# Kernel optimization log

Hardware: AMD Instinct MI355X
Metric: run time of the kernel (lower is better)

## Reference

```python
import jax, jax.numpy as jnp
import numpy as np

B, S, D = 4, 2048, 512
H = 8
DEPTH = D // H  # 64


def setup_inputs() -> dict:
    key = jax.random.key(0)
    ks = jax.random.split(key, 6)
    scale = 1.0 / np.sqrt(D)
    return {
        "x": jax.random.normal(ks[0], (B, S, D), dtype=jnp.float32),
        "y": jax.random.normal(ks[1], (B, S, D), dtype=jnp.float32),
        "W_q": jax.random.normal(ks[2], (D, D), dtype=jnp.float32) * scale,
        "W_k": jax.random.normal(ks[3], (D, D), dtype=jnp.float32) * scale,
        "W_v": jax.random.normal(ks[4], (D, D), dtype=jnp.float32) * scale,
        "W_o": jax.random.normal(ks[5], (D, D), dtype=jnp.float32) * scale,
    }


def _split_heads(t):
    # [B, S, D] -> [B, H, S, DEPTH]
    b, s, _ = t.shape
    return t.reshape(b, s, H, DEPTH).transpose(0, 2, 1, 3)


def reference(x, y, W_q, W_k, W_v, W_o):
    q = _split_heads(x @ W_q) * (DEPTH ** -0.5)   # [B,H,Sq,d]
    k = _split_heads(y @ W_k)                      # [B,H,Sk,d]
    v = _split_heads(y @ W_v)                      # [B,H,Sk,d]
    logits = jnp.einsum("bhqd,bhkd->bhqk", q, k)   # [B,H,Sq,Sk]
    weights = jax.nn.softmax(logits, axis=-1)
    attn = jnp.einsum("bhqk,bhkd->bhqd", weights, v)  # [B,H,Sq,d]
    attn = attn.transpose(0, 2, 1, 3).reshape(x.shape[0], x.shape[1], D)
    return attn @ W_o
```

## Files before the change

kernel.cpp:

```cpp
#include <hip/hip_runtime.h>
#include <hip/hip_bf16.h>
#include <math.h>
#include <stdint.h>

#define NB 4
#define NS 2048
#define ND 512
#define NH 8
#define DEP 64
#define KVHALF (NS / 2)

typedef __attribute__((ext_vector_type(8))) short bf16x8;
typedef __attribute__((ext_vector_type(4))) short bf16x4;
typedef __attribute__((ext_vector_type(4))) float f32x4;
typedef __attribute__((ext_vector_type(16))) float f32x16;

#define QSCALE 0.18033688011112042f

__device__ __forceinline__ short f2b(float f) {
  unsigned u = __float_as_uint(f);
  u += 0x7FFF + ((u >> 16) & 1);
  return (short)(u >> 16);
}
__device__ __forceinline__ unsigned pk2(float a, float b) {
  union { __hip_bfloat162 h; unsigned u; } c;
  c.h = __float22bfloat162_rn(float2{a, b});
  return c.u;
}
__device__ __forceinline__ void dma16(const void* g, void* l) {
  __builtin_amdgcn_global_load_lds(
      (const __attribute__((address_space(1))) void*)g,
      (__attribute__((address_space(3))) void*)l, 16, 0, 0);
}

__global__ __launch_bounds__(256) void prep(
    const float* __restrict__ x, const float* __restrict__ y,
    const float* __restrict__ W0, const float* __restrict__ W1,
    const float* __restrict__ W2, const float* __restrict__ W3,
    short* __restrict__ xb, short* __restrict__ yb, short* __restrict__ T0,
    short* __restrict__ T1, short* __restrict__ T2, short* __restrict__ T3) {
  const int t = threadIdx.x;
  if (blockIdx.y < 2) {
    const float* src = blockIdx.y ? y : x;
    short* dst = blockIdx.y ? yb : xb;
    size_t i = ((size_t)blockIdx.x * 256 + t) * 4;
    float4 v = *(const float4*)(src + i);
    bf16x4 o;
    o[0] = f2b(v.x); o[1] = f2b(v.y); o[2] = f2b(v.z); o[3] = f2b(v.w);
    *(bf16x4*)(dst + i) = o;
    return;
  }
  const int bx = blockIdx.x;
  if (bx >= 256) return;
  const int wj = bx >> 6, rem = bx & 63;
  const float* W = wj == 0 ? W0 : wj == 1 ? W1 : wj == 2 ? W2 : W3;
  short* T = wj == 0 ? T0 : wj == 1 ? T1 : wj == 2 ? T2 : T3;
  __shared__ float tile[64][65];
  const int k0 = (rem >> 3) * 64, n0 = (rem & 7) * 64;
#pragma unroll
  for (int i = 0; i < 4; ++i) {
    int r = (t >> 4) + i * 16;
    int c = (t & 15) * 4;
    float4 v = *(const float4*)&W[(size_t)(k0 + r) * ND + n0 + c];
    tile[r][c] = v.x; tile[r][c + 1] = v.y;
    tile[r][c + 2] = v.z; tile[r][c + 3] = v.w;
  }
  __syncthreads();
#pragma unroll
  for (int i = 0; i < 4; ++i) {
    int n = (t >> 4) + i * 16;
    int kc = (t & 15) * 4;
    bf16x4 o;
#pragma unroll
    for (int j = 0; j < 4; ++j) o[j] = f2b(tile[kc + j][n]);
    *(bf16x4*)&T[(size_t)(n0 + n) * ND + k0 + kc] = o;
  }
}

__device__ __forceinline__ void gemm128(const short* __restrict__ A,
                                        const short* __restrict__ Bt,
                                        short* __restrict__ Cout, int mode,
                                        float alpha) {
  __shared__ short As[128 * 64];
  __shared__ short Bs[128 * 64];
  const int t = threadIdx.x;
  const int wave = t >> 6, lane = t & 63;
  const int m = lane & 15, quad = lane >> 4;
  const int m0 = blockIdx.y * 128, n0 = blockIdx.x * 128;
  const int mh = (wave >> 1) * 64, nh = (wave & 1) * 64;
  const int r8 = lane >> 3;
  const int c8 = (lane & 7) ^ r8;
  const int mx7 = m & 7;
  f32x4 acc[4][4];
#pragma unroll
  for (int i = 0; i < 4; ++i)
#pragma unroll
    for (int j = 0; j < 4; ++j) acc[i][j] = (f32x4){0.f, 0.f, 0.f, 0.f};

  for (int k0 = 0; k0 < ND; k0 += 64) {
    __syncthreads();
#pragma unroll
    for (int i = 0; i < 4; ++i) {
      int row = i * 32 + wave * 8 + r8;
      dma16(A + (size_t)(m0 + row) * ND + k0 + c8 * 8,
            As + (i * 256 + wave * 64) * 8);
      dma16(Bt + (size_t)(n0 + row) * ND + k0 + c8 * 8,
            Bs + (i * 256 + wave * 64) * 8);
    }
    __syncthreads();
    bf16x8 af[4][2], bf[4][2];
#pragma unroll
    for (int mt = 0; mt < 4; ++mt)
#pragma unroll
      for (int kc = 0; kc < 2; ++kc)
        af[mt][kc] = *(const bf16x8*)(As + (mh + mt * 16 + m) * 64 +
                                      ((kc * 4 + quad) ^ mx7) * 8);
#pragma unroll
    for (int nt = 0; nt < 4; ++nt)
#pragma unroll
      for (int kc = 0; kc < 2; ++kc)
        bf[nt][kc] = *(const bf16x8*)(Bs + (nh + nt * 16 + m) * 64 +
                                      ((kc * 4 + quad) ^ mx7) * 8);
#pragma unroll
    for (int mt = 0; mt < 4; ++mt)
#pragma unroll
      for (int nt = 0; nt < 4; ++nt)
#pragma unroll
        for (int kc = 0; kc < 2; ++kc)
          acc[mt][nt] = __builtin_amdgcn_mfma_f32_16x16x32_bf16(
              af[mt][kc], bf[nt][kc], acc[mt][nt], 0, 0, 0);
  }
  if (mode == 2) {
#pragma unroll
    for (int mt = 0; mt < 4; ++mt)
#pragma unroll
      for (int nt = 0; nt < 4; ++nt) {
        int row0 = m0 + mh + mt * 16 + quad * 4;
        int col = n0 + nh + nt * 16 + m;
        int b_ = row0 >> 11, s_ = row0 & (NS - 1);
        int h_ = col >> 6, d_ = col & (DEP - 1);
        uint2 p;
        p.x = pk2(acc[mt][nt][0] * alpha, acc[mt][nt][1] * alpha);
        p.y = pk2(acc[mt][nt][2] * alpha, acc[mt][nt][3] * alpha);
        *(uint2*)(Cout + (size_t)((b_ * NH + h_) * DEP + d_) * NS + s_) = p;
      }
  } else {
#pragma unroll
    for (int mt = 0; mt < 4; ++mt)
#pragma unroll
      for (int nt = 0; nt < 4; ++nt)
#pragma unroll
        for (int r = 0; r < 4; ++r) {
          int row = m0 + mh + mt * 16 + quad * 4 + r;
          int col = n0 + nh + nt * 16 + m;
          Cout[(size_t)row * ND + col] = f2b(acc[mt][nt][r] * alpha);
        }
  }
}

__global__ __launch_bounds__(256) void qkv_gemm(
    const short* __restrict__ xb, const short* __restrict__ yb,
    const short* __restrict__ Wqt, const short* __restrict__ Wkt,
    const short* __restrict__ Wvt, short* __restrict__ Qb,
    short* __restrict__ Kb, short* __restrict__ Vtb) {
  if (blockIdx.z == 0)
    gemm128(xb, Wqt, Qb, 1, QSCALE);
  else if (blockIdx.z == 1)
    gemm128(yb, Wkt, Kb, 1, 1.0f);
  else
    gemm128(yb, Wvt, Vtb, 2, 1.0f);
}

__global__ __launch_bounds__(256) void out_gemm(const short* __restrict__ A,
                                                const short* __restrict__ Bt,
                                                float* __restrict__ Cout) {
  __shared__ short As[2][128 * 64];
  __shared__ short Bs[2][64 * 64];
  const int t = threadIdx.x;
  const int wave = t >> 6, lane = t & 63;
  const int m = lane & 15, quad = lane >> 4;
  const int m0 = blockIdx.y * 128, n0 = blockIdx.x * 64;
  const int mh = (wave >> 1) * 64, nh = (wave & 1) * 32;
  const int r8 = lane >> 3;
  const int c8 = (lane & 7) ^ r8;
  const int mx7 = m & 7;
  f32x4 acc[4][2];
#pragma unroll
  for (int i = 0; i < 4; ++i)
#pragma unroll
    for (int j = 0; j < 2; ++j) acc[i][j] = (f32x4){0.f, 0.f, 0.f, 0.f};

#pragma unroll
  for (int i = 0; i < 4; ++i)
    dma16(A + (size_t)(m0 + i * 32 + wave * 8 + r8) * ND + c8 * 8,
          As[0] + (i * 256 + wave * 64) * 8);
#pragma unroll
  for (int i = 0; i < 2; ++i)
    dma16(Bt + (size_t)(n0 + i * 32 + wave * 8 + r8) * ND + c8 * 8,
          Bs[0] + (i * 256 + wave * 64) * 8);

  int buf = 0;
  for (int k0 = 0; k0 < ND; k0 += 64, buf ^= 1) {
    __syncthreads();
    if (k0 + 64 < ND) {
#pragma unroll
      for (int i = 0; i < 4; ++i)
        dma16(A + (size_t)(m0 + i * 32 + wave * 8 + r8) * ND + k0 + 64 + c8 * 8,
              As[buf ^ 1] + (i * 256 + wave * 64) * 8);
#pragma unroll
      for (int i = 0; i < 2; ++i)
        dma16(Bt + (size_t)(n0 + i * 32 + wave * 8 + r8) * ND + k0 + 64 +
                  c8 * 8,
              Bs[buf ^ 1] + (i * 256 + wave * 64) * 8);
    }
    bf16x8 af[4][2], bf[2][2];
#pragma unroll
    for (int mt = 0; mt < 4; ++mt)
#pragma unroll
      for (int kc = 0; kc < 2; ++kc)
        af[mt][kc] = *(const bf16x8*)(As[buf] + (mh + mt * 16 + m) * 64 +
                                      ((kc * 4 + quad) ^ mx7) * 8);
#pragma unroll
    for (int nt = 0; nt < 2; ++nt)
#pragma unroll
      for (int kc = 0; kc < 2; ++kc)
        bf[nt][kc] = *(const bf16x8*)(Bs[buf] + (nh + nt * 16 + m) * 64 +
                                      ((kc * 4 + quad) ^ mx7) * 8);
#pragma unroll
    for (int mt = 0; mt < 4; ++mt)
#pragma unroll
      for (int nt = 0; nt < 2; ++nt)
#pragma unroll
        for (int kc = 0; kc < 2; ++kc)
          acc[mt][nt] = __builtin_amdgcn_mfma_f32_16x16x32_bf16(
              af[mt][kc], bf[nt][kc], acc[mt][nt], 0, 0, 0);
  }
#pragma unroll
  for (int mt = 0; mt < 4; ++mt)
#pragma unroll
    for (int nt = 0; nt < 2; ++nt)
#pragma unroll
      for (int r = 0; r < 4; ++r) {
        int row = m0 + mh + mt * 16 + quad * 4 + r;
        int col = n0 + nh + nt * 16 + m;
        Cout[(size_t)row * ND + col] = acc[mt][nt][r];
      }
}

__global__ __launch_bounds__(512, 4) void attn_mfma(
    const short* __restrict__ Qb, const short* __restrict__ Kb,
    const short* __restrict__ Vtb, short* __restrict__ Ob) {
  __shared__ short Ks[2][2][64 * 64];
  __shared__ short Vts[2][2][64 * 64];
  const int t = threadIdx.x;
  const int wave = t >> 6, lane = t & 63;
  const int zh = wave >> 2, wl = wave & 3;
  const int l31 = lane & 31, hi = lane >> 5;
  const int sw = lane & 7;
  const int bh = blockIdx.y, b = bh >> 3, h = bh & 7;
  const int q0 = blockIdx.x * 128 + wl * 32;
  const int kvb = zh * KVHALF;
  const size_t rowb = (size_t)b * NS;
  const short* Vtbase = Vtb + (size_t)(bh * DEP) * NS;
  const int r8 = lane >> 3;
  const int c8 = (lane & 7) ^ r8;

  bf16x8 qf[4];
#pragma unroll
  for (int dc = 0; dc < 4; ++dc)
    qf[dc] = *(const bf16x8*)(Qb + (rowb + q0 + l31) * ND + h * DEP + dc * 16 +
                              hi * 8);

  f32x16 kzero;
#pragma unroll
  for (int i = 0; i < 16; ++i) kzero[i] = 0.f;

  float l_ = 0.0f;
  f32x16 Ot[2];
#pragma unroll
  for (int dt = 0; dt < 2; ++dt)
#pragma unroll
    for (int i = 0; i < 16; ++i) Ot[dt][i] = 0.f;

#pragma unroll
  for (int i = 0; i < 2; ++i) {
    int row = i * 32 + wl * 8 + r8;
    dma16(Kb + (rowb + kvb + row) * ND + h * DEP + c8 * 8,
          &Ks[zh][0][(i * 256 + wl * 64) * 8]);
    dma16(Vtbase + (size_t)row * NS + kvb + c8 * 8,
          &Vts[zh][0][(i * 256 + wl * 64) * 8]);
  }

  int buf = 0;
  for (int kv0 = 0; kv0 < KVHALF; kv0 += 64, buf ^= 1) {
    __syncthreads();
    if (kv0 + 64 < KVHALF) {
#pragma unroll
      for (int i = 0; i < 2; ++i) {
        int row = i * 32 + wl * 8 + r8;
        dma16(Kb + (rowb + kvb + kv0 + 64 + row) * ND + h * DEP + c8 * 8,
              &Ks[zh][buf ^ 1][(i * 256 + wl * 64) * 8]);
        dma16(Vtbase + (size_t)row * NS + kvb + kv0 + 64 + c8 * 8,
              &Vts[zh][buf ^ 1][(i * 256 + wl * 64) * 8]);
      }
    }

    f32x16 St[2];
#pragma unroll
    for (int kt = 0; kt < 2; ++kt) {
      bf16x8 kf0 = *(const bf16x8*)(&Ks[zh][buf][(kt * 32 + l31) * 64 +
                                                 (hi ^ sw) * 8]);
      St[kt] = __builtin_amdgcn_mfma_f32_32x32x16_bf16(kf0, qf[0], kzero,
                                                       0, 0, 0);
#pragma unroll
      for (int dc = 1; dc < 4; ++dc) {
        bf16x8 kf = *(const bf16x8*)(&Ks[zh][buf][(kt * 32 + l31) * 64 +
                                                  ((dc * 2 + hi) ^ sw) * 8]);
        St[kt] = __builtin_amdgcn_mfma_f32_32x32x16_bf16(kf, qf[dc], St[kt],
                                                         0, 0, 0);
      }
    }

    bf16x8 pf[4];
    float rs = 0.f;
#pragma unroll
    for (int s = 0; s < 4; ++s) {
      const int kt = s >> 1, base = (s & 1) * 8;
      float E[8];
#pragma unroll
      for (int j = 0; j < 8; ++j) {
        E[j] = __builtin_amdgcn_exp2f(St[kt][base + j]);
      }
      rs += ((E[0] + E[1]) + (E[2] + E[3])) + ((E[4] + E[5]) + (E[6] + E[7]));
      unsigned A0 = pk2(E[0], E[1]), A1 = pk2(E[2], E[3]);
      unsigned A2 = pk2(E[4], E[5]), A3 = pk2(E[6], E[7]);
      auto r02 =
          __builtin_amdgcn_permlane32_swap((int)A0, (int)A2, false, false);
      auto r13 =
          __builtin_amdgcn_permlane32_swap((int)A1, (int)A3, false, false);
      union { bf16x8 v; int u[4]; } pu;
      pu.u[0] = r02[0]; pu.u[1] = r13[0]; pu.u[2] = r02[1]; pu.u[3] = r13[1];
      pf[s] = pu.v;
    }
    l_ += rs;

#pragma unroll
    for (int dt = 0; dt < 2; ++dt)
#pragma unroll
      for (int s = 0; s < 4; ++s) {
        bf16x8 vf = *(const bf16x8*)(&Vts[zh][buf][(dt * 32 + l31) * 64 +
                                                   ((s * 2 + hi) ^ sw) * 8]);
        Ot[dt] = __builtin_amdgcn_mfma_f32_32x32x16_bf16(vf, pf[s], Ot[dt],
                                                         0, 0, 0);
      }
  }

  l_ += __shfl_xor(l_, 32, 64);

  __syncthreads();
  float* Ox = (float*)Ks;
  float* lx = (float*)Vts;
  if (zh == 1) {
#pragma unroll
    for (int dt = 0; dt < 2; ++dt)
#pragma unroll
      for (int r = 0; r < 16; ++r) {
        int d = dt * 32 + (r & 3) + 8 * (r >> 2) + 4 * hi;
        Ox[(wl * 64 + d) * 32 + l31] = Ot[dt][r];
      }
    if (lane < 32) lx[wl * 32 + l31] = l_;
  }
  __syncthreads();
  if (zh == 0) {
    float linv = 1.0f / (l_ + lx[wl * 32 + l31]);
    size_t row = rowb + q0 + l31;
#pragma unroll
    for (int dt = 0; dt < 2; ++dt)
#pragma unroll
      for (int g = 0; g < 4; ++g) {
        int d0 = dt * 32 + g * 8 + hi * 4;
        float o[4];
#pragma unroll
        for (int j = 0; j < 4; ++j)
          o[j] = Ot[dt][g * 4 + j] + Ox[(wl * 64 + d0 + j) * 32 + l31];
        uint2 pk;
        pk.x = pk2(o[0] * linv, o[1] * linv);
        pk.y = pk2(o[2] * linv, o[3] * linv);
        *(uint2*)(Ob + row * ND + h * DEP + d0) = pk;
      }
  }
}

extern "C" void kernel_launch(void* const* d_in, const int* in_sizes, int n_in,
                              void* d_out, int out_size, void* d_ws,
                              size_t ws_size, hipStream_t stream) {
  const float* x = (const float*)d_in[0];
  const float* y = (const float*)d_in[1];
  const float* Wq = (const float*)d_in[2];
  const float* Wk = (const float*)d_in[3];
  const float* Wv = (const float*)d_in[4];
  const float* Wo = (const float*)d_in[5];
  float* out = (float*)d_out;

  const size_t mat = (size_t)NB * NS * ND;
  const size_t wsz = (size_t)ND * ND;
  short* xb = (short*)d_ws;
  short* yb = xb + mat;
  short* Wqt = yb + mat;
  short* Wkt = Wqt + wsz;
  short* Wvt = Wkt + wsz;
  short* Wot = Wvt + wsz;
  short* Qb = Wot + wsz;
  short* Kb = Qb + mat;
  short* Vtb = Kb + mat;
  short* attnb = xb;

  prep<<<dim3(mat / 1024, 3), 256, 0, stream>>>(x, y, Wq, Wk, Wv, Wo, xb, yb,
                                                Wqt, Wkt, Wvt, Wot);
  qkv_gemm<<<dim3(ND / 128, (NB * NS) / 128, 3), 256, 0, stream>>>(
      xb, yb, Wqt, Wkt, Wvt, Qb, Kb, Vtb);
  attn_mfma<<<dim3(NS / 128, NB * NH), 512, 0, stream>>>(Qb, Kb, Vtb, attnb);
  out_gemm<<<dim3(ND / 64, (NB * NS) / 128), 256, 0, stream>>>(attnb, Wot,
                                                               out);
}
```

Before: 184.3 us.

## Software-pipeline QK of the next tile with softmax and PV of the previous tile

Restructures the attention KV loop into a two-stage software pipeline. The QK^T MFMAs for tile t run in the same stage as the exp/pack and PV MFMAs for tile t-1, using two alternating score register sets. K and V DMA loads are staggered by one tile. MFMA sections are wrapped in s_setprio so matrix work is favoured over other waves. The aim is to hide exp and LDS latency behind matrix work and overlap loads with compute, at the cost of more live registers and lower occupancy.

```diff
diff --git a/kernel.cpp b/kernel.cpp
--- a/kernel.cpp
+++ b/kernel.cpp
@@ -9,6 +9,7 @@
 #define NH 8
 #define DEP 64
 #define KVHALF (NS / 2)
+#define NT (KVHALF / 64)
 
 typedef __attribute__((ext_vector_type(8))) short bf16x8;
 typedef __attribute__((ext_vector_type(4))) short bf16x4;
@@ -282,45 +283,43 @@
 #pragma unroll
     for (int i = 0; i < 16; ++i) Ot[dt][i] = 0.f;
 
-#pragma unroll
-  for (int i = 0; i < 2; ++i) {
-    int row = i * 32 + wl * 8 + r8;
-    dma16(Kb + (rowb + kvb + row) * ND + h * DEP + c8 * 8,
-          &Ks[zh][0][(i * 256 + wl * 64) * 8]);
-    dma16(Vtbase + (size_t)row * NS + kvb + c8 * 8,
-          &Vts[zh][0][(i * 256 + wl * 64) * 8]);
-  }
-
-  int buf = 0;
-  for (int kv0 = 0; kv0 < KVHALF; kv0 += 64, buf ^= 1) {
-    __syncthreads();
-    if (kv0 + 64 < KVHALF) {
-#pragma unroll
-      for (int i = 0; i < 2; ++i) {
-        int row = i * 32 + wl * 8 + r8;
-        dma16(Kb + (rowb + kvb + kv0 + 64 + row) * ND + h * DEP + c8 * 8,
-              &Ks[zh][buf ^ 1][(i * 256 + wl * 64) * 8]);
-        dma16(Vtbase + (size_t)row * NS + kvb + kv0 + 64 + c8 * 8,
-              &Vts[zh][buf ^ 1][(i * 256 + wl * 64) * 8]);
-      }
-    }
-
-    f32x16 St[2];
+  f32x16 StA[2], StB[2];
+
+  auto KDMA = [&](int tt) {
+#pragma unroll
+    for (int i = 0; i < 2; ++i) {
+      int row = i * 32 + wl * 8 + r8;
+      dma16(Kb + (rowb + kvb + tt * 64 + row) * ND + h * DEP + c8 * 8,
+            &Ks[zh][tt & 1][(i * 256 + wl * 64) * 8]);
+    }
+  };
+  auto VDMA = [&](int tt) {
+#pragma unroll
+    for (int i = 0; i < 2; ++i) {
+      int row = i * 32 + wl * 8 + r8;
+      dma16(Vtbase + (size_t)row * NS + kvb + tt * 64 + c8 * 8,
+            &Vts[zh][tt & 1][(i * 256 + wl * 64) * 8]);
+    }
+  };
+  auto QK = [&](int tt, f32x16 (&Sc)[2]) {
+    const short* kb = &Ks[zh][tt & 1][0];
+    __builtin_amdgcn_s_setprio(1);
 #pragma unroll
     for (int kt = 0; kt < 2; ++kt) {
-      bf16x8 kf0 = *(const bf16x8*)(&Ks[zh][buf][(kt * 32 + l31) * 64 +
-                                                 (hi ^ sw) * 8]);
-      St[kt] = __builtin_amdgcn_mfma_f32_32x32x16_bf16(kf0, qf[0], kzero,
+      bf16x8 kf0 = *(const bf16x8*)(kb + (kt * 32 + l31) * 64 + (hi ^ sw) * 8);
+      Sc[kt] = __builtin_amdgcn_mfma_f32_32x32x16_bf16(kf0, qf[0], kzero,
                                                        0, 0, 0);
 #pragma unroll
       for (int dc = 1; dc < 4; ++dc) {
-        bf16x8 kf = *(const bf16x8*)(&Ks[zh][buf][(kt * 32 + l31) * 64 +
-                                                  ((dc * 2 + hi) ^ sw) * 8]);
-        St[kt] = __builtin_amdgcn_mfma_f32_32x32x16_bf16(kf, qf[dc], St[kt],
+        bf16x8 kf = *(const bf16x8*)(kb + (kt * 32 + l31) * 64 +
+                                     ((dc * 2 + hi) ^ sw) * 8);
+        Sc[kt] = __builtin_amdgcn_mfma_f32_32x32x16_bf16(kf, qf[dc], Sc[kt],
                                                          0, 0, 0);
       }
     }
-
+    __builtin_amdgcn_s_setprio(0);
+  };
+  auto SMPV = [&](int tt, const f32x16 (&Sp)[2]) {
     bf16x8 pf[4];
     float rs = 0.f;
 #pragma unroll
@@ -329,7 +328,7 @@
       float E[8];
 #pragma unroll
       for (int j = 0; j < 8; ++j) {
-        E[j] = __builtin_amdgcn_exp2f(St[kt][base + j]);
+        E[j] = __builtin_amdgcn_exp2f(Sp[kt][base + j]);
       }
       rs += ((E[0] + E[1]) + (E[2] + E[3])) + ((E[4] + E[5]) + (E[6] + E[7]));
       unsigned A0 = pk2(E[0], E[1]), A1 = pk2(E[2], E[3]);
@@ -343,17 +342,48 @@
       pf[s] = pu.v;
     }
     l_ += rs;
-
+    const short* vb = &Vts[zh][tt & 1][0];
+    __builtin_amdgcn_s_setprio(1);
 #pragma unroll
     for (int dt = 0; dt < 2; ++dt)
 #pragma unroll
       for (int s = 0; s < 4; ++s) {
-        bf16x8 vf = *(const bf16x8*)(&Vts[zh][buf][(dt * 32 + l31) * 64 +
-                                                   ((s * 2 + hi) ^ sw) * 8]);
+        bf16x8 vf = *(const bf16x8*)(vb + (dt * 32 + l31) * 64 +
+                                     ((s * 2 + hi) ^ sw) * 8);
         Ot[dt] = __builtin_amdgcn_mfma_f32_32x32x16_bf16(vf, pf[s], Ot[dt],
                                                          0, 0, 0);
       }
-  }
+    __builtin_amdgcn_s_setprio(0);
+  };
+
+  KDMA(0);
+  {
+    __syncthreads();
+    KDMA(1);
+    VDMA(0);
+    QK(0, StA);
+  }
+  for (int j = 0; j < 7; ++j) {
+    const int t1 = 2 * j + 1, t2 = 2 * j + 2;
+    __syncthreads();
+    KDMA(t1 + 1);
+    VDMA(t1);
+    QK(t1, StB);
+    SMPV(t1 - 1, StA);
+    __syncthreads();
+    KDMA(t2 + 1);
+    VDMA(t2);
+    QK(t2, StA);
+    SMPV(t2 - 1, StB);
+  }
+  {
+    __syncthreads();
+    VDMA(15);
+    QK(15, StB);
+    SMPV(14, StA);
+  }
+  __syncthreads();
+  SMPV(15, StB);
 
   l_ += __shfl_xor(l_, 32, 64);
 
```

New measurement: 222.7 us. 1.21x slower.

## Software-pipeline attention loop: overlap QK of next tile with PV of previous

Applied to the files above, without the earlier changes.

Restructures the KV loop of the attention kernel into a skewed software pipeline. Each step issues QK^T for tile t while doing PV for tile t-1, and K and V DMA loads are staggered by one tile. It also raises wave priority around the MFMA blocks with s_setprio. The goal is to hide the softmax exp/pack latency and the LDS loads behind matrix-core work, at the cost of higher register pressure from the double P fragment buffers and a hard-coded tile count of 16.

```diff
diff --git a/kernel.cpp b/kernel.cpp
--- a/kernel.cpp
+++ b/kernel.cpp
@@ -282,78 +282,118 @@
 #pragma unroll
     for (int i = 0; i < 16; ++i) Ot[dt][i] = 0.f;
 
-#pragma unroll
-  for (int i = 0; i < 2; ++i) {
-    int row = i * 32 + wl * 8 + r8;
-    dma16(Kb + (rowb + kvb + row) * ND + h * DEP + c8 * 8,
-          &Ks[zh][0][(i * 256 + wl * 64) * 8]);
-    dma16(Vtbase + (size_t)row * NS + kvb + c8 * 8,
-          &Vts[zh][0][(i * 256 + wl * 64) * 8]);
-  }
-
-  int buf = 0;
-  for (int kv0 = 0; kv0 < KVHALF; kv0 += 64, buf ^= 1) {
-    __syncthreads();
-    if (kv0 + 64 < KVHALF) {
-#pragma unroll
-      for (int i = 0; i < 2; ++i) {
-        int row = i * 32 + wl * 8 + r8;
-        dma16(Kb + (rowb + kvb + kv0 + 64 + row) * ND + h * DEP + c8 * 8,
-              &Ks[zh][buf ^ 1][(i * 256 + wl * 64) * 8]);
-        dma16(Vtbase + (size_t)row * NS + kvb + kv0 + 64 + c8 * 8,
-              &Vts[zh][buf ^ 1][(i * 256 + wl * 64) * 8]);
-      }
-    }
-
-    f32x16 St[2];
-#pragma unroll
-    for (int kt = 0; kt < 2; ++kt) {
-      bf16x8 kf0 = *(const bf16x8*)(&Ks[zh][buf][(kt * 32 + l31) * 64 +
-                                                 (hi ^ sw) * 8]);
-      St[kt] = __builtin_amdgcn_mfma_f32_32x32x16_bf16(kf0, qf[0], kzero,
-                                                       0, 0, 0);
-#pragma unroll
-      for (int dc = 1; dc < 4; ++dc) {
-        bf16x8 kf = *(const bf16x8*)(&Ks[zh][buf][(kt * 32 + l31) * 64 +
-                                                  ((dc * 2 + hi) ^ sw) * 8]);
-        St[kt] = __builtin_amdgcn_mfma_f32_32x32x16_bf16(kf, qf[dc], St[kt],
-                                                         0, 0, 0);
-      }
-    }
-
-    bf16x8 pf[4];
-    float rs = 0.f;
-#pragma unroll
-    for (int s = 0; s < 4; ++s) {
-      const int kt = s >> 1, base = (s & 1) * 8;
-      float E[8];
-#pragma unroll
-      for (int j = 0; j < 8; ++j) {
-        E[j] = __builtin_amdgcn_exp2f(St[kt][base + j]);
-      }
-      rs += ((E[0] + E[1]) + (E[2] + E[3])) + ((E[4] + E[5]) + (E[6] + E[7]));
-      unsigned A0 = pk2(E[0], E[1]), A1 = pk2(E[2], E[3]);
-      unsigned A2 = pk2(E[4], E[5]), A3 = pk2(E[6], E[7]);
-      auto r02 =
-          __builtin_amdgcn_permlane32_swap((int)A0, (int)A2, false, false);
-      auto r13 =
-          __builtin_amdgcn_permlane32_swap((int)A1, (int)A3, false, false);
-      union { bf16x8 v; int u[4]; } pu;
-      pu.u[0] = r02[0]; pu.u[1] = r13[0]; pu.u[2] = r02[1]; pu.u[3] = r13[1];
-      pf[s] = pu.v;
-    }
-    l_ += rs;
-
-#pragma unroll
-    for (int dt = 0; dt < 2; ++dt)
-#pragma unroll
-      for (int s = 0; s < 4; ++s) {
-        bf16x8 vf = *(const bf16x8*)(&Vts[zh][buf][(dt * 32 + l31) * 64 +
-                                                   ((s * 2 + hi) ^ sw) * 8]);
-        Ot[dt] = __builtin_amdgcn_mfma_f32_32x32x16_bf16(vf, pf[s], Ot[dt],
-                                                         0, 0, 0);
-      }
-  }
+  f32x16 St0, St1;
+  bf16x8 pfA[4], pfB[4];
+
+#define KDMA(tt)                                                          \
+  {                                                                       \
+    _Pragma("unroll") for (int i_ = 0; i_ < 2; ++i_) {                    \
+      int row_ = i_ * 32 + wl * 8 + r8;                                   \
+      dma16(Kb + (rowb + kvb + (tt) * 64 + row_) * ND + h * DEP + c8 * 8, \
+            &Ks[zh][(tt) & 1][(i_ * 256 + wl * 64) * 8]);                 \
+    }                                                                     \
+  }
+#define VDMA(tt)                                                       \
+  {                                                                    \
+    _Pragma("unroll") for (int i_ = 0; i_ < 2; ++i_) {                 \
+      int row_ = i_ * 32 + wl * 8 + r8;                                \
+      dma16(Vtbase + (size_t)row_ * NS + kvb + (tt) * 64 + c8 * 8,     \
+            &Vts[zh][(tt) & 1][(i_ * 256 + wl * 64) * 8]);             \
+    }                                                                  \
+  }
+#define QKH(SD, KT, kb_)                                                     \
+  {                                                                          \
+    bf16x8 kf_;                                                              \
+    kf_ = *(const bf16x8*)((kb_) + ((KT)*32 + l31) * 64 + ((0 + hi) ^ sw) * 8); \
+    SD = __builtin_amdgcn_mfma_f32_32x32x16_bf16(kf_, qf[0], kzero, 0, 0, 0); \
+    kf_ = *(const bf16x8*)((kb_) + ((KT)*32 + l31) * 64 + ((2 + hi) ^ sw) * 8); \
+    SD = __builtin_amdgcn_mfma_f32_32x32x16_bf16(kf_, qf[1], SD, 0, 0, 0);   \
+    kf_ = *(const bf16x8*)((kb_) + ((KT)*32 + l31) * 64 + ((4 + hi) ^ sw) * 8); \
+    SD = __builtin_amdgcn_mfma_f32_32x32x16_bf16(kf_, qf[2], SD, 0, 0, 0);   \
+    kf_ = *(const bf16x8*)((kb_) + ((KT)*32 + l31) * 64 + ((6 + hi) ^ sw) * 8); \
+    SD = __builtin_amdgcn_mfma_f32_32x32x16_bf16(kf_, qf[3], SD, 0, 0, 0);   \
+  }
+#define QK(tt)                                  \
+  {                                             \
+    const short* kb_ = &Ks[zh][(tt) & 1][0];    \
+    __builtin_amdgcn_s_setprio(1);              \
+    QKH(St0, 0, kb_);                           \
+    QKH(St1, 1, kb_);                           \
+    __builtin_amdgcn_s_setprio(0);              \
+  }
+#define SM_SLICE(SS, BASE, SIDX, PF)                                         \
+  {                                                                          \
+    float E0 = __builtin_amdgcn_exp2f(SS[(BASE) + 0]);                       \
+    float E1 = __builtin_amdgcn_exp2f(SS[(BASE) + 1]);                       \
+    float E2 = __builtin_amdgcn_exp2f(SS[(BASE) + 2]);                       \
+    float E3 = __builtin_amdgcn_exp2f(SS[(BASE) + 3]);                       \
+    float E4 = __builtin_amdgcn_exp2f(SS[(BASE) + 4]);                       \
+    float E5 = __builtin_amdgcn_exp2f(SS[(BASE) + 5]);                       \
+    float E6 = __builtin_amdgcn_exp2f(SS[(BASE) + 6]);                       \
+    float E7 = __builtin_amdgcn_exp2f(SS[(BASE) + 7]);                       \
+    l_ += ((E0 + E1) + (E2 + E3)) + ((E4 + E5) + (E6 + E7));                 \
+    unsigned A0 = pk2(E0, E1), A1 = pk2(E2, E3);                             \
+    unsigned A2 = pk2(E4, E5), A3 = pk2(E6, E7);                             \
+    auto r02 =                                                               \
+        __builtin_amdgcn_permlane32_swap((int)A0, (int)A2, false, false);    \
+    auto r13 =                                                               \
+        __builtin_amdgcn_permlane32_swap((int)A1, (int)A3, false, false);    \
+    union { bf16x8 v; int u[4]; } pu_;                                       \
+    pu_.u[0] = r02[0]; pu_.u[1] = r13[0]; pu_.u[2] = r02[1];                 \
+    pu_.u[3] = r13[1];                                                       \
+    PF[SIDX] = pu_.v;                                                        \
+  }
+#define SM(PF)                  \
+  SM_SLICE(St0, 0, 0, PF)       \
+  SM_SLICE(St0, 8, 1, PF)       \
+  SM_SLICE(St1, 0, 2, PF)       \
+  SM_SLICE(St1, 8, 3, PF)
+#define PV(tt, PF)                                                         \
+  {                                                                        \
+    const short* vb_ = &Vts[zh][(tt) & 1][0];                              \
+    __builtin_amdgcn_s_setprio(1);                                         \
+    _Pragma("unroll") for (int dt_ = 0; dt_ < 2; ++dt_) {                  \
+      _Pragma("unroll") for (int s_ = 0; s_ < 4; ++s_) {                   \
+        bf16x8 vf_ = *(const bf16x8*)(vb_ + (dt_ * 32 + l31) * 64 +        \
+                                      ((s_ * 2 + hi) ^ sw) * 8);           \
+        Ot[dt_] = __builtin_amdgcn_mfma_f32_32x32x16_bf16(vf_, PF[s_],     \
+                                                          Ot[dt_], 0, 0, 0); \
+      }                                                                    \
+    }                                                                      \
+    __builtin_amdgcn_s_setprio(0);                                         \
+  }
+
+  KDMA(0);
+  __syncthreads();
+  KDMA(1);
+  VDMA(0);
+  QK(0);
+  SM(pfA);
+#pragma unroll 1
+  for (int j = 0; j < 7; ++j) {
+    const int t1 = 2 * j + 1, t2 = 2 * j + 2;
+    __syncthreads();
+    KDMA(t1 + 1);
+    VDMA(t1);
+    QK(t1);
+    PV(t1 - 1, pfA);
+    SM(pfB);
+    __syncthreads();
+    KDMA(t2 + 1);
+    VDMA(t2);
+    QK(t2);
+    PV(t2 - 1, pfB);
+    SM(pfA);
+  }
+  {
+    __syncthreads();
+    VDMA(15);
+    QK(15);
+    PV(14, pfA);
+    SM(pfB);
+  }
+  __syncthreads();
+  PV(15, pfB);
 
   l_ += __shfl_xor(l_, 32, 64);
 
@@ -381,14 +421,21 @@
         int d0 = dt * 32 + g * 8 + hi * 4;
         float o[4];
 #pragma unroll
-        for (int j = 0; j < 4; ++j)
-          o[j] = Ot[dt][g * 4 + j] + Ox[(wl * 64 + d0 + j) * 32 + l31];
+        for (int jj = 0; jj < 4; ++jj)
+          o[jj] = Ot[dt][g * 4 + jj] + Ox[(wl * 64 + d0 + jj) * 32 + l31];
         uint2 pk;
         pk.x = pk2(o[0] * linv, o[1] * linv);
         pk.y = pk2(o[2] * linv, o[3] * linv);
         *(uint2*)(Ob + row * ND + h * DEP + d0) = pk;
       }
   }
+#undef KDMA
+#undef VDMA
+#undef QKH
+#undef QK
+#undef SM_SLICE
+#undef SM
+#undef PV
 }
 
 extern "C" void kernel_launch(void* const* d_in, const int* in_sizes, int n_in,
```

Result: slower. 207.0 us (+12.3%).
